# Performance work log

Measured on AMD Instinct MI355X. Metric: run time of the kernel, lower is better.

## Reference

```python
import jax, jax.numpy as jnp
import numpy as np

B, D = 65536, 365

def _linp(k, fan_in, fan_out):
    # torch nn.Linear default init: U(-1/sqrt(fan_in), 1/sqrt(fan_in))
    kw, kb = jax.random.split(k)
    bound = 1.0 / np.sqrt(fan_in)
    W = jax.random.uniform(kw, (fan_in, fan_out), jnp.float32, -bound, bound)
    b = jax.random.uniform(kb, (fan_out,), jnp.float32, -bound, bound)
    return W, b

def setup_inputs() -> dict:
    key = jax.random.key(0)
    ks = jax.random.split(key, 9)
    x = jax.random.normal(ks[0], (B, D), jnp.float32)
    W1, b1 = _linp(ks[1], D, 512)
    W2, b2 = _linp(ks[2], 512, 256)
    W3, b3 = _linp(ks[3], 256, 128)
    Ws, bs = _linp(ks[4], 6, 32)
    Wc1, bc1 = _linp(ks[5], 128 + 32, 64)
    Wc2, bc2 = _linp(ks[6], 64, 32)
    Wc3, bc3 = _linp(ks[7], 32, 1)
    return dict(x=x, W1=W1, b1=b1, W2=W2, b2=b2, W3=W3, b3=b3,
                Ws=Ws, bs=bs, Wc1=Wc1, bc1=bc1, Wc2=Wc2, bc2=bc2,
                Wc3=Wc3, bc3=bc3)

def _row_stats(x):
    # fused row-wise moments: mean, std (ddof=1), min, max, skew, kurtosis
    mu = jnp.mean(x, axis=1, keepdims=True)          # [B,1]
    c = x - mu                                        # [B,D]
    var1 = jnp.sum(c * c, axis=1) / (x.shape[1] - 1)  # unbiased, matches torch.std()
    sigma = jnp.sqrt(var1)
    m3 = jnp.mean(c ** 3, axis=1)
    m4 = jnp.mean(c ** 4, axis=1)
    skew = m3 / (sigma ** 3 + 1e-8)
    kurt = m4 / (sigma ** 4 + 1e-8)
    return jnp.stack([mu[:, 0], sigma, jnp.min(x, axis=1), jnp.max(x, axis=1), skew, kurt], axis=1)

def reference(x, W1, b1, W2, b2, W3, b3, Ws, bs, Wc1, bc1, Wc2, bc2, Wc3, bc3):
    h = jax.nn.relu(x @ W1 + b1)
    h = jax.nn.relu(h @ W2 + b2)
    seq = jax.nn.relu(h @ W3 + b3)            # [B,128]
    stat = _row_stats(x) @ Ws + bs            # [B,32]
    comb = jnp.concatenate([seq, stat], axis=1)
    c = jax.nn.relu(comb @ Wc1 + bc1)
    c = jax.nn.relu(c @ Wc2 + bc2)
    out = jax.nn.sigmoid(c @ Wc3 + bc3)       # [B,1]
    return out[:, 0]
```

## Files before the change

kernel.cpp:

```cpp
#include <hip/hip_runtime.h>
#include <math.h>

typedef __attribute__((ext_vector_type(8)))  short short8;
typedef __attribute__((ext_vector_type(16))) float float16;

#define DEVI __device__ __forceinline__

DEVI short f2bf(float f) {
    unsigned u = __float_as_uint(f);
    u = (u + 0x7fffu + ((u >> 16) & 1u)) >> 16;
    return (short)u;
}
DEVI unsigned pk2(float a, float b) {
    return (unsigned)(unsigned short)f2bf(a) | ((unsigned)(unsigned short)f2bf(b) << 16);
}
DEVI float16 mfma16(short8 a, short8 b, float16 c) {
    return __builtin_amdgcn_mfma_f32_32x32x16_bf16(a, b, c, 0, 0, 0);
}
DEVI int rowof(int r, int h) { return (r & 3) + 8 * (r >> 2) + 4 * h; }

__global__ void prep_weights(const float* __restrict__ W1, const float* __restrict__ W2,
                             const float* __restrict__ W3, const float* __restrict__ Wc1,
                             const float* __restrict__ Wc2, short* __restrict__ ws) {
    int idx = blockIdx.x * 256 + threadIdx.x;
    const float* src; int K, N, kpad, local, base;
    if (idx < 196608)      { base = 0;      local = idx;          K = 365; N = 512; kpad = 384; src = W1;  }
    else if (idx < 327680) { base = 196608; local = idx - 196608; K = 512; N = 256; kpad = 512; src = W2;  }
    else if (idx < 360448) { base = 327680; local = idx - 327680; K = 256; N = 128; kpad = 256; src = W3;  }
    else if (idx < 370688) { base = 360448; local = idx - 360448; K = 160; N = 64;  kpad = 160; src = Wc1; }
    else                   { base = 370688; local = idx - 370688; K = 64;  N = 32;  kpad = 64;  src = Wc2; }
    int n = local / kpad, kp = local - n * kpad;
    float v = (kp < K) ? src[kp * N + n] : 0.0f;
    ws[base + local] = f2bf(v);
}

__global__ __launch_bounds__(512, 2)
void fused_mlp(const float* __restrict__ x,
               const float* __restrict__ b1f, const float* __restrict__ b2f,
               const float* __restrict__ b3f, const float* __restrict__ Wsf,
               const float* __restrict__ bsf, const float* __restrict__ bc1f,
               const float* __restrict__ bc2f, const float* __restrict__ Wc3f,
               const float* __restrict__ bc3f,
               const short* __restrict__ W1t, const short* __restrict__ W2t,
               const short* __restrict__ W3t, const short* __restrict__ Wc1t,
               const short* __restrict__ Wc2t, float* __restrict__ out)
{
    __shared__ __align__(16) char smem[63488];
    short* AB0  = (short*)(smem);
    short* AB1  = (short*)(smem + 8192);
    short* SB0  = (short*)(smem + 16384);
    short* SB1  = (short*)(smem + 34816);
    short* C1s  = (short*)(smem + 16384);
    float* C2s  = (float*)(smem + 34816);
    short* FEAT = (short*)(smem + 53248);

    const int tid  = (int)threadIdx.x;
    const int lane = tid & 63;
    const int wave = tid >> 6;
    const int m    = lane & 31;
    const int h    = lane >> 5;
    const int rowBase = (int)blockIdx.x * 128;

    const int xr = tid >> 2;
    const int xo = (tid & 3) ^ (xr & 3);
    const float* xrow = x + (size_t)(rowBase + xr) * 365;

    float s1 = 0.f, s2 = 0.f, s3 = 0.f, s4 = 0.f, mn = 1e30f, mx = -1e30f;
    unsigned sxd[48];
    unsigned parkH1[64];
    unsigned park2[32];
    unsigned park3[16];

    auto issue_x = [&](int c, float* xf) {
        #pragma unroll
        for (int j = 0; j < 8; ++j) {
            int col = c * 32 + xo * 8 + j;
            xf[j] = (col < 365) ? xrow[col] : 0.f;
        }
    };
    auto mom_stash = [&](int c, const float* xf) {
        #pragma unroll
        for (int q = 0; q < 4; ++q) sxd[c * 4 + q] = pk2(xf[2 * q], xf[2 * q + 1]);
        #pragma unroll
        for (int j = 0; j < 8; ++j) {
            int col = c * 32 + xo * 8 + j;
            if (col < 365) {
                float v = xf[j], v2 = v * v;
                s1 += v; s2 += v2; s3 += v2 * v; s4 += v2 * v2;
                mn = fminf(mn, v); mx = fmaxf(mx, v);
            }
        }
    };
    auto write_a = [&](int c, short* A) {
        int4 w4;
        w4.x = (int)sxd[c * 4 + 0]; w4.y = (int)sxd[c * 4 + 1];
        w4.z = (int)sxd[c * 4 + 2]; w4.w = (int)sxd[c * 4 + 3];
        *(int4*)(A + tid * 8) = w4;
    };
    auto ldA = [&](const short* A, int mt, int ks) -> short8 {
        int a16 = (mt * 32 + m) * 4 + ((ks * 2 + h) ^ (m & 3));
        return *(const short8*)(A + a16 * 8);
    };
    auto ldS = [&](const short* S, int stride, int mt, int k0) -> short8 {
        return *(const short8*)(S + (mt * 32 + m) * stride + k0 + h * 8);
    };

    float16 A0, A1, A2, A3;
    #pragma unroll
    for (int i = 0; i < 16; ++i) { A0[i] = 0.f; A1[i] = 0.f; A2[i] = 0.f; A3[i] = 0.f; }
    float xfa[8], xfb[8];

    {
        const short* B1 = W1t + (wave * 32 + m) * 384 + h * 8;
        issue_x(0, xfa); issue_x(1, xfb);
        mom_stash(0, xfa);
        write_a(0, AB0);
        short8 bq0 = *(const short8*)(B1);
        short8 bq1 = *(const short8*)(B1 + 16);
        __syncthreads();
        #pragma unroll
        for (int c = 0; c < 12; ++c) {
            const short* Acur = (c & 1) ? AB1 : AB0;
            short*       Anxt = (c & 1) ? AB0 : AB1;
            if (c + 2 < 12) issue_x(c + 2, (c & 1) ? xfb : xfa);
            short8 nb0 = bq0, nb1 = bq1;
            if (c + 1 < 12) {
                nb0 = *(const short8*)(B1 + (c + 1) * 32);
                nb1 = *(const short8*)(B1 + (c + 1) * 32 + 16);
            }
            short8 a;
            a = ldA(Acur, 0, 0); A0 = mfma16(a, bq0, A0);
            a = ldA(Acur, 1, 0); A1 = mfma16(a, bq0, A1);
            a = ldA(Acur, 2, 0); A2 = mfma16(a, bq0, A2);
            a = ldA(Acur, 3, 0); A3 = mfma16(a, bq0, A3);
            a = ldA(Acur, 0, 1); A0 = mfma16(a, bq1, A0);
            a = ldA(Acur, 1, 1); A1 = mfma16(a, bq1, A1);
            a = ldA(Acur, 2, 1); A2 = mfma16(a, bq1, A2);
            a = ldA(Acur, 3, 1); A3 = mfma16(a, bq1, A3);
            if (c + 1 < 12) {
                mom_stash(c + 1, (c & 1) ? xfa : xfb);
                write_a(c + 1, Anxt);
            }
            bq0 = nb0; bq1 = nb1;
            __syncthreads();
        }
        float bb = b1f[wave * 32 + m];
        #pragma unroll
        for (int rr = 0; rr < 8; ++rr) {
            parkH1[rr]      = pk2(fmaxf(A0[2*rr] + bb, 0.f), fmaxf(A0[2*rr+1] + bb, 0.f));
            parkH1[8 + rr]  = pk2(fmaxf(A1[2*rr] + bb, 0.f), fmaxf(A1[2*rr+1] + bb, 0.f));
            parkH1[16 + rr] = pk2(fmaxf(A2[2*rr] + bb, 0.f), fmaxf(A2[2*rr+1] + bb, 0.f));
            parkH1[24 + rr] = pk2(fmaxf(A3[2*rr] + bb, 0.f), fmaxf(A3[2*rr+1] + bb, 0.f));
        }
    }

    {
        #pragma unroll
        for (int off = 1; off <= 2; off <<= 1) {
            s1 += __shfl_xor(s1, off); s2 += __shfl_xor(s2, off);
            s3 += __shfl_xor(s3, off); s4 += __shfl_xor(s4, off);
            mn = fminf(mn, __shfl_xor(mn, off)); mx = fmaxf(mx, __shfl_xor(mx, off));
        }
        float mean  = s1 * (1.0f / 365.0f);
        float var1  = (s2 - 365.0f * mean * mean) * (1.0f / 364.0f);
        float sigma = sqrtf(var1);
        float m3 = (s3 - 3.0f * mean * s2) * (1.0f / 365.0f) + 2.0f * mean * mean * mean;
        float mm = mean * mean;
        float m4 = (s4 - 4.0f * mean * s3 + 6.0f * mm * s2) * (1.0f / 365.0f) - 3.0f * mm * mm;
        float sg2 = sigma * sigma;
        float skew = m3 / (sigma * sg2 + 1e-8f);
        float kurt = m4 / (sg2 * sg2 + 1e-8f);
        float st[6] = { mean, sigma, mn, mx, skew, kurt };
        #pragma unroll
        for (int nn = 0; nn < 8; nn += 2) {
            int n0 = (tid & 3) * 8 + nn;
            float f0 = bsf[n0], f1 = bsf[n0 + 1];
            #pragma unroll
            for (int j = 0; j < 6; ++j) { f0 += st[j] * Wsf[j * 32 + n0]; f1 += st[j] * Wsf[j * 32 + n0 + 1]; }
            *(unsigned*)(FEAT + xr * 40 + n0) = pk2(f0, f1);
        }
    }

    {
        const short* B1 = W1t + ((8 + wave) * 32 + m) * 384 + h * 8;
        #pragma unroll
        for (int i = 0; i < 16; ++i) { A0[i] = 0.f; A1[i] = 0.f; A2[i] = 0.f; A3[i] = 0.f; }
        write_a(0, AB0);
        short8 bq0 = *(const short8*)(B1);
        short8 bq1 = *(const short8*)(B1 + 16);
        __syncthreads();
        #pragma unroll
        for (int c = 0; c < 12; ++c) {
            const short* Acur = (c & 1) ? AB1 : AB0;
            short*       Anxt = (c & 1) ? AB0 : AB1;
            short8 nb0 = bq0, nb1 = bq1;
            if (c + 1 < 12) {
                nb0 = *(const short8*)(B1 + (c + 1) * 32);
                nb1 = *(const short8*)(B1 + (c + 1) * 32 + 16);
            }
            short8 a;
            a = ldA(Acur, 0, 0); A0 = mfma16(a, bq0, A0);
            a = ldA(Acur, 1, 0); A1 = mfma16(a, bq0, A1);
            a = ldA(Acur, 2, 0); A2 = mfma16(a, bq0, A2);
            a = ldA(Acur, 3, 0); A3 = mfma16(a, bq0, A3);
            a = ldA(Acur, 0, 1); A0 = mfma16(a, bq1, A0);
            a = ldA(Acur, 1, 1); A1 = mfma16(a, bq1, A1);
            a = ldA(Acur, 2, 1); A2 = mfma16(a, bq1, A2);
            a = ldA(Acur, 3, 1); A3 = mfma16(a, bq1, A3);
            if (c + 1 < 12) write_a(c + 1, Anxt);
            bq0 = nb0; bq1 = nb1;
            __syncthreads();
        }
        float bb = b1f[(8 + wave) * 32 + m];
        #pragma unroll
        for (int rr = 0; rr < 8; ++rr) {
            parkH1[32 + rr]      = pk2(fmaxf(A0[2*rr] + bb, 0.f), fmaxf(A0[2*rr+1] + bb, 0.f));
            parkH1[32 + 8 + rr]  = pk2(fmaxf(A1[2*rr] + bb, 0.f), fmaxf(A1[2*rr+1] + bb, 0.f));
            parkH1[32 + 16 + rr] = pk2(fmaxf(A2[2*rr] + bb, 0.f), fmaxf(A2[2*rr+1] + bb, 0.f));
            parkH1[32 + 24 + rr] = pk2(fmaxf(A3[2*rr] + bb, 0.f), fmaxf(A3[2*rr+1] + bb, 0.f));
        }
    }

    float16 H0, H1, H2, H3;
    #pragma unroll
    for (int i = 0; i < 16; ++i) { H0[i] = 0.f; H1[i] = 0.f; H2[i] = 0.f; H3[i] = 0.f; }
    {
        const short* B2 = W2t + (wave * 32 + m) * 512 + h * 8;
        auto wS = [&](int c, short* S) {
            int lo = (2 * c) & 7;
            int pb = (c < 4) ? 0 : 32;
            if (wave == lo || wave == lo + 1) {
                int col = (wave - lo) * 32 + m;
                #pragma unroll
                for (int mt = 0; mt < 4; ++mt)
                #pragma unroll
                for (int rr = 0; rr < 8; ++rr) {
                    unsigned pv = parkH1[pb + mt * 8 + rr];
                    S[(mt * 32 + rowof(2 * rr,     h)) * 72 + col] = (short)(pv & 0xffffu);
                    S[(mt * 32 + rowof(2 * rr + 1, h)) * 72 + col] = (short)(pv >> 16);
                }
            }
        };
        wS(0, SB0);
        short8 cb[4], nb[4];
        #pragma unroll
        for (int ks = 0; ks < 4; ++ks) cb[ks] = *(const short8*)(B2 + ks * 16);
        __syncthreads();
        #pragma unroll
        for (int c = 0; c < 8; ++c) {
            const short* Scur = (c & 1) ? SB1 : SB0;
            short*       Snxt = (c & 1) ? SB0 : SB1;
            if (c + 1 < 8) {
                wS(c + 1, Snxt);
                #pragma unroll
                for (int ks = 0; ks < 4; ++ks) nb[ks] = *(const short8*)(B2 + (c + 1) * 64 + ks * 16);
            }
            #pragma unroll
            for (int ks = 0; ks < 4; ++ks) {
                short8 a;
                a = ldS(Scur, 72, 0, ks * 16); H0 = mfma16(a, cb[ks], H0);
                a = ldS(Scur, 72, 1, ks * 16); H1 = mfma16(a, cb[ks], H1);
                a = ldS(Scur, 72, 2, ks * 16); H2 = mfma16(a, cb[ks], H2);
                a = ldS(Scur, 72, 3, ks * 16); H3 = mfma16(a, cb[ks], H3);
            }
            if (c + 1 < 8) {
                #pragma unroll
                for (int ks = 0; ks < 4; ++ks) cb[ks] = nb[ks];
            }
            __syncthreads();
        }
        float bb = b2f[wave * 32 + m];
        #pragma unroll
        for (int rr = 0; rr < 8; ++rr) {
            park2[rr]      = pk2(fmaxf(H0[2*rr] + bb, 0.f), fmaxf(H0[2*rr+1] + bb, 0.f));
            park2[8 + rr]  = pk2(fmaxf(H1[2*rr] + bb, 0.f), fmaxf(H1[2*rr+1] + bb, 0.f));
            park2[16 + rr] = pk2(fmaxf(H2[2*rr] + bb, 0.f), fmaxf(H2[2*rr+1] + bb, 0.f));
            park2[24 + rr] = pk2(fmaxf(H3[2*rr] + bb, 0.f), fmaxf(H3[2*rr+1] + bb, 0.f));
        }
    }

    float16 Sq0, Sq1;
    #pragma unroll
    for (int i = 0; i < 16; ++i) { Sq0[i] = 0.f; Sq1[i] = 0.f; }
    {
        int nt3 = wave >> 1, mtb = 2 * (wave & 1);
        const short* B3 = W3t + (nt3 * 32 + m) * 256 + h * 8;
        auto wS3 = [&](int c, short* S) {
            int lo = 2 * c;
            if (wave == lo || wave == lo + 1) {
                int col = (wave - lo) * 32 + m;
                #pragma unroll
                for (int mt = 0; mt < 4; ++mt)
                #pragma unroll
                for (int rr = 0; rr < 8; ++rr) {
                    unsigned pv = park2[mt * 8 + rr];
                    S[(mt * 32 + rowof(2 * rr,     h)) * 72 + col] = (short)(pv & 0xffffu);
                    S[(mt * 32 + rowof(2 * rr + 1, h)) * 72 + col] = (short)(pv >> 16);
                }
            }
        };
        wS3(0, SB0);
        short8 cb[4], nb[4];
        #pragma unroll
        for (int ks = 0; ks < 4; ++ks) cb[ks] = *(const short8*)(B3 + ks * 16);
        __syncthreads();
        #pragma unroll
        for (int c = 0; c < 4; ++c) {
            const short* Scur = (c & 1) ? SB1 : SB0;
            short*       Snxt = (c & 1) ? SB0 : SB1;
            if (c + 1 < 4) {
                wS3(c + 1, Snxt);
                #pragma unroll
                for (int ks = 0; ks < 4; ++ks) nb[ks] = *(const short8*)(B3 + (c + 1) * 64 + ks * 16);
            }
            #pragma unroll
            for (int ks = 0; ks < 4; ++ks) {
                short8 a;
                a = ldS(Scur, 72, mtb,     ks * 16); Sq0 = mfma16(a, cb[ks], Sq0);
                a = ldS(Scur, 72, mtb + 1, ks * 16); Sq1 = mfma16(a, cb[ks], Sq1);
            }
            if (c + 1 < 4) {
                #pragma unroll
                for (int ks = 0; ks < 4; ++ks) cb[ks] = nb[ks];
            }
            __syncthreads();
        }
        float bb = b3f[nt3 * 32 + m];
        #pragma unroll
        for (int rr = 0; rr < 8; ++rr) {
            park3[rr]     = pk2(fmaxf(Sq0[2*rr] + bb, 0.f), fmaxf(Sq0[2*rr+1] + bb, 0.f));
            park3[8 + rr] = pk2(fmaxf(Sq1[2*rr] + bb, 0.f), fmaxf(Sq1[2*rr+1] + bb, 0.f));
        }
    }

    {
        int mt4 = wave & 3, nt4 = wave >> 2;
        const short* B4 = Wc1t + (nt4 * 32 + m) * 160 + h * 8;
        float bb = bc1f[nt4 * 32 + m];
        float16 Cv;
        #pragma unroll
        for (int i = 0; i < 16; ++i) Cv[i] = 0.f;
        auto wS4 = [&](int c, short* S) {
            if ((wave >> 2) == c) {
                int col = ((wave >> 1) & 1) * 32 + m;
                #pragma unroll
                for (int jj = 0; jj < 2; ++jj)
                #pragma unroll
                for (int rr = 0; rr < 8; ++rr) {
                    unsigned pv = park3[jj * 8 + rr];
                    int mt = 2 * (wave & 1) + jj;
                    S[(mt * 32 + rowof(2 * rr,     h)) * 72 + col] = (short)(pv & 0xffffu);
                    S[(mt * 32 + rowof(2 * rr + 1, h)) * 72 + col] = (short)(pv >> 16);
                }
            }
        };
        wS4(0, SB0); wS4(1, SB1);
        __syncthreads();
        #pragma unroll
        for (int ks = 0; ks < 4; ++ks) {
            short8 a = ldS(SB0, 72, mt4, ks * 16);
            short8 b = *(const short8*)(B4 + ks * 16);
            Cv = mfma16(a, b, Cv);
        }
        #pragma unroll
        for (int ks = 0; ks < 4; ++ks) {
            short8 a = ldS(SB1, 72, mt4, ks * 16);
            short8 b = *(const short8*)(B4 + 64 + ks * 16);
            Cv = mfma16(a, b, Cv);
        }
        #pragma unroll
        for (int ks = 0; ks < 2; ++ks) {
            short8 a = ldS(FEAT, 40, mt4, ks * 16);
            short8 b = *(const short8*)(B4 + 128 + ks * 16);
            Cv = mfma16(a, b, Cv);
        }
        __syncthreads();
        #pragma unroll
        for (int rr = 0; rr < 8; ++rr) {
            C1s[(mt4 * 32 + rowof(2 * rr,     h)) * 72 + nt4 * 32 + m] = f2bf(fmaxf(Cv[2*rr]   + bb, 0.f));
            C1s[(mt4 * 32 + rowof(2 * rr + 1, h)) * 72 + nt4 * 32 + m] = f2bf(fmaxf(Cv[2*rr+1] + bb, 0.f));
        }
        __syncthreads();
    }

    {
        if (wave < 4) {
            const short* B5 = Wc2t + m * 64 + h * 8;
            float bb = bc2f[m];
            float16 Cv;
            #pragma unroll
            for (int i = 0; i < 16; ++i) Cv[i] = 0.f;
            #pragma unroll
            for (int ks = 0; ks < 4; ++ks) {
                short8 a = ldS(C1s, 72, wave, ks * 16);
                short8 b = *(const short8*)(B5 + ks * 16);
                Cv = mfma16(a, b, Cv);
            }
            #pragma unroll
            for (int rr = 0; rr < 16; ++rr)
                C2s[(wave * 32 + rowof(rr, h)) * 33 + m] = fmaxf(Cv[rr] + bb, 0.f);
        }
        __syncthreads();
    }

    if (tid < 128) {
        float z = bc3f[0];
        #pragma unroll
        for (int i = 0; i < 32; ++i) z += C2s[tid * 33 + i] * Wc3f[i];
        out[rowBase + tid] = 1.0f / (1.0f + expf(-z));
    }
}

extern "C" void kernel_launch(void* const* d_in, const int* in_sizes, int n_in,
                              void* d_out, int out_size, void* d_ws, size_t ws_size,
                              hipStream_t stream)
{
    (void)in_sizes; (void)n_in; (void)out_size; (void)ws_size;
    const float* x   = (const float*)d_in[0];
    const float* W1  = (const float*)d_in[1];
    const float* b1  = (const float*)d_in[2];
    const float* W2  = (const float*)d_in[3];
    const float* b2  = (const float*)d_in[4];
    const float* W3  = (const float*)d_in[5];
    const float* b3  = (const float*)d_in[6];
    const float* Ws  = (const float*)d_in[7];
    const float* bs  = (const float*)d_in[8];
    const float* Wc1 = (const float*)d_in[9];
    const float* bc1 = (const float*)d_in[10];
    const float* Wc2 = (const float*)d_in[11];
    const float* bc2 = (const float*)d_in[12];
    const float* Wc3 = (const float*)d_in[13];
    const float* bc3 = (const float*)d_in[14];
    short* ws = (short*)d_ws;

    prep_weights<<<1456, 256, 0, stream>>>(W1, W2, W3, Wc1, Wc2, ws);
    fused_mlp<<<512, 512, 0, stream>>>(x, b1, b2, b3, Ws, bs, bc1, bc2, Wc3, bc3,
                                       ws, ws + 196608, ws + 327680, ws + 360448, ws + 370688,
                                       (float*)d_out);
}
```

Baseline: 238.2 us.

## Rewrite fused MLP with 64-row tiles, K-chunked weight layout, and interleaved layer streaming

Replaces the fused kernel with a new version that processes 64 rows per block instead of 128 and doubles the grid. The whole bf16 x tile is staged in LDS up front, and layer 1 and layer 2 are interleaved in 128-column slabs so hidden activations never need to be parked in registers. The weight prep kernel now writes a K-chunked (16-wide) transposed layout through an LDS transpose for coalesced stores. Occupancy is targeted higher via launch_bounds(512,4), at the cost of more redundant weight reads per row and more barriers.

```diff
diff --git a/kernel.cpp b/kernel.cpp
--- a/kernel.cpp
+++ b/kernel.cpp
@@ -18,149 +18,114 @@
     return __builtin_amdgcn_mfma_f32_32x32x16_bf16(a, b, c, 0, 0, 0);
 }
 DEVI int rowof(int r, int h) { return (r & 3) + 8 * (r >> 2) + 4 * h; }
-
-__global__ void prep_weights(const float* __restrict__ W1, const float* __restrict__ W2,
-                             const float* __restrict__ W3, const float* __restrict__ Wc1,
-                             const float* __restrict__ Wc2, short* __restrict__ ws) {
-    int idx = blockIdx.x * 256 + threadIdx.x;
-    const float* src; int K, N, kpad, local, base;
-    if (idx < 196608)      { base = 0;      local = idx;          K = 365; N = 512; kpad = 384; src = W1;  }
-    else if (idx < 327680) { base = 196608; local = idx - 196608; K = 512; N = 256; kpad = 512; src = W2;  }
-    else if (idx < 360448) { base = 327680; local = idx - 327680; K = 256; N = 128; kpad = 256; src = W3;  }
-    else if (idx < 370688) { base = 360448; local = idx - 360448; K = 160; N = 64;  kpad = 160; src = Wc1; }
-    else                   { base = 370688; local = idx - 370688; K = 64;  N = 32;  kpad = 64;  src = Wc2; }
-    int n = local / kpad, kp = local - n * kpad;
-    float v = (kp < K) ? src[kp * N + n] : 0.0f;
-    ws[base + local] = f2bf(v);
-}
-
-__global__ __launch_bounds__(512, 2)
-void fused_mlp(const float* __restrict__ x,
-               const float* __restrict__ b1f, const float* __restrict__ b2f,
-               const float* __restrict__ b3f, const float* __restrict__ Wsf,
-               const float* __restrict__ bsf, const float* __restrict__ bc1f,
-               const float* __restrict__ bc2f, const float* __restrict__ Wc3f,
-               const float* __restrict__ bc3f,
-               const short* __restrict__ W1t, const short* __restrict__ W2t,
-               const short* __restrict__ W3t, const short* __restrict__ Wc1t,
-               const short* __restrict__ Wc2t, float* __restrict__ out)
+DEVI short8 lds8(const short* p) { return *(const short8*)p; }
+
+#define W1T_OFF  0
+#define W2T_OFF  188416
+#define W3T_OFF  319488
+#define WC1T_OFF 352256
+#define WC2T_OFF 362496
+
+__global__ void prep_v2(const float* __restrict__ W1, const float* __restrict__ W2,
+                        const float* __restrict__ W3, const float* __restrict__ Wc1,
+                        const float* __restrict__ Wc2, short* __restrict__ ws) {
+    __shared__ short T[16 * 72];
+    int b = blockIdx.x, t = threadIdx.x;
+    const float* src; int K, N; size_t base; int kc, nb;
+    if (b < 184)        {            src = W1;  K = 365; N = 512; base = W1T_OFF;  kc = b >> 3;  nb = b & 7; }
+    else if (b < 312)   { int l = b - 184; src = W2;  K = 512; N = 256; base = W2T_OFF;  kc = l >> 2;  nb = l & 3; }
+    else if (b < 344)   { int l = b - 312; src = W3;  K = 256; N = 128; base = W3T_OFF;  kc = l >> 1;  nb = l & 1; }
+    else if (b < 354)   {            src = Wc1; K = 160; N = 64;  base = WC1T_OFF; kc = b - 344; nb = 0; }
+    else                {            src = Wc2; K = 64;  N = 32;  base = WC2T_OFF; kc = b - 354; nb = 0; }
+    int n = nb * 64 + (t & 63);
+    int kr = t >> 6;
+    #pragma unroll
+    for (int i = 0; i < 4; ++i) {
+        int krow = kr + 4 * i;
+        int k = kc * 16 + krow;
+        float v = (k < K && n < N) ? src[(size_t)k * N + n] : 0.f;
+        T[krow * 72 + (t & 63)] = f2bf(v);
+    }
+    __syncthreads();
+    int n2 = t >> 2, ksq = (t & 3) * 4;
+    int ng = nb * 64 + n2;
+    if (ng < N) {
+        unsigned lo = (unsigned)(unsigned short)T[ksq * 72 + n2]
+                    | ((unsigned)(unsigned short)T[(ksq + 1) * 72 + n2] << 16);
+        unsigned hi = (unsigned)(unsigned short)T[(ksq + 2) * 72 + n2]
+                    | ((unsigned)(unsigned short)T[(ksq + 3) * 72 + n2] << 16);
+        uint2 d; d.x = lo; d.y = hi;
+        *(uint2*)(ws + base + ((size_t)kc * N + ng) * 16 + ksq) = d;
+    }
+}
+
+__global__ __launch_bounds__(512, 4)
+void fused_v2(const float* __restrict__ x,
+              const float* __restrict__ b1f, const float* __restrict__ b2f,
+              const float* __restrict__ b3f, const float* __restrict__ Wsf,
+              const float* __restrict__ bsf, const float* __restrict__ bc1f,
+              const float* __restrict__ bc2f, const float* __restrict__ Wc3f,
+              const float* __restrict__ bc3f,
+              const short* __restrict__ wsw, float* __restrict__ out)
 {
-    __shared__ __align__(16) char smem[63488];
-    short* AB0  = (short*)(smem);
-    short* AB1  = (short*)(smem + 8192);
-    short* SB0  = (short*)(smem + 16384);
-    short* SB1  = (short*)(smem + 34816);
-    short* C1s  = (short*)(smem + 16384);
-    float* C2s  = (float*)(smem + 34816);
-    short* FEAT = (short*)(smem + 53248);
+    __shared__ __align__(16) char smem[65536];
+    short* XT    = (short*)smem;
+    short* SB    = (short*)(smem + 48128);
+    short* C1    = (short*)smem;
+    short* FEATL = (short*)(smem + 12288);
+    float* C2    = (float*)(smem + 20480);
+
+    const short* W1t  = wsw + W1T_OFF;
+    const short* W2t  = wsw + W2T_OFF;
+    const short* W3t  = wsw + W3T_OFF;
+    const short* Wc1t = wsw + WC1T_OFF;
+    const short* Wc2t = wsw + WC2T_OFF;
 
     const int tid  = (int)threadIdx.x;
     const int lane = tid & 63;
-    const int wave = tid >> 6;
+    const int wv   = tid >> 6;
     const int m    = lane & 31;
     const int h    = lane >> 5;
-    const int rowBase = (int)blockIdx.x * 128;
-
-    const int xr = tid >> 2;
-    const int xo = (tid & 3) ^ (xr & 3);
-    const float* xrow = x + (size_t)(rowBase + xr) * 365;
-
+    const int mt   = wv & 1;
+    const int nl   = wv >> 1;
+    const int rowBase = (int)blockIdx.x * 64;
+
+    const int r0 = tid >> 3, j0 = tid & 7;
+    const float* xrow = x + (size_t)(rowBase + r0) * 365;
     float s1 = 0.f, s2 = 0.f, s3 = 0.f, s4 = 0.f, mn = 1e30f, mx = -1e30f;
-    unsigned sxd[48];
-    unsigned parkH1[64];
-    unsigned park2[32];
-    unsigned park3[16];
-
-    auto issue_x = [&](int c, float* xf) {
-        #pragma unroll
-        for (int j = 0; j < 8; ++j) {
-            int col = c * 32 + xo * 8 + j;
-            xf[j] = (col < 365) ? xrow[col] : 0.f;
-        }
-    };
-    auto mom_stash = [&](int c, const float* xf) {
-        #pragma unroll
-        for (int q = 0; q < 4; ++q) sxd[c * 4 + q] = pk2(xf[2 * q], xf[2 * q + 1]);
-        #pragma unroll
-        for (int j = 0; j < 8; ++j) {
-            int col = c * 32 + xo * 8 + j;
-            if (col < 365) {
-                float v = xf[j], v2 = v * v;
-                s1 += v; s2 += v2; s3 += v2 * v; s4 += v2 * v2;
-                mn = fminf(mn, v); mx = fmaxf(mx, v);
-            }
-        }
-    };
-    auto write_a = [&](int c, short* A) {
-        int4 w4;
-        w4.x = (int)sxd[c * 4 + 0]; w4.y = (int)sxd[c * 4 + 1];
-        w4.z = (int)sxd[c * 4 + 2]; w4.w = (int)sxd[c * 4 + 3];
-        *(int4*)(A + tid * 8) = w4;
-    };
-    auto ldA = [&](const short* A, int mt, int ks) -> short8 {
-        int a16 = (mt * 32 + m) * 4 + ((ks * 2 + h) ^ (m & 3));
-        return *(const short8*)(A + a16 * 8);
-    };
-    auto ldS = [&](const short* S, int stride, int mt, int k0) -> short8 {
-        return *(const short8*)(S + (mt * 32 + m) * stride + k0 + h * 8);
-    };
-
-    float16 A0, A1, A2, A3;
-    #pragma unroll
-    for (int i = 0; i < 16; ++i) { A0[i] = 0.f; A1[i] = 0.f; A2[i] = 0.f; A3[i] = 0.f; }
-    float xfa[8], xfb[8];
-
+    #pragma unroll
+    for (int i = 0; i < 6; ++i) {
+        int o = j0 + 8 * i;
+        if (o <= 45) {
+            float xf[8];
+            #pragma unroll
+            for (int jj = 0; jj < 8; ++jj) {
+                int col = o * 8 + jj;
+                xf[jj] = (col < 365) ? xrow[col] : 0.f;
+            }
+            #pragma unroll
+            for (int jj = 0; jj < 8; ++jj) {
+                int col = o * 8 + jj;
+                if (col < 365) {
+                    float v = xf[jj], v2 = v * v;
+                    s1 += v; s2 += v2; s3 += v2 * v; s4 += v2 * v2;
+                    mn = fminf(mn, v); mx = fmaxf(mx, v);
+                }
+            }
+            int4 w4;
+            w4.x = (int)pk2(xf[0], xf[1]); w4.y = (int)pk2(xf[2], xf[3]);
+            w4.z = (int)pk2(xf[4], xf[5]); w4.w = (int)pk2(xf[6], xf[7]);
+            *(int4*)(XT + r0 * 376 + o * 8) = w4;
+        }
+    }
+    #pragma unroll
+    for (int off = 1; off <= 4; off <<= 1) {
+        s1 += __shfl_xor(s1, off); s2 += __shfl_xor(s2, off);
+        s3 += __shfl_xor(s3, off); s4 += __shfl_xor(s4, off);
+        mn = fminf(mn, __shfl_xor(mn, off)); mx = fmaxf(mx, __shfl_xor(mx, off));
+    }
+    unsigned fdw0, fdw1;
     {
-        const short* B1 = W1t + (wave * 32 + m) * 384 + h * 8;
-        issue_x(0, xfa); issue_x(1, xfb);
-        mom_stash(0, xfa);
-        write_a(0, AB0);
-        short8 bq0 = *(const short8*)(B1);
-        short8 bq1 = *(const short8*)(B1 + 16);
-        __syncthreads();
-        #pragma unroll
-        for (int c = 0; c < 12; ++c) {
-            const short* Acur = (c & 1) ? AB1 : AB0;
-            short*       Anxt = (c & 1) ? AB0 : AB1;
-            if (c + 2 < 12) issue_x(c + 2, (c & 1) ? xfb : xfa);
-            short8 nb0 = bq0, nb1 = bq1;
-            if (c + 1 < 12) {
-                nb0 = *(const short8*)(B1 + (c + 1) * 32);
-                nb1 = *(const short8*)(B1 + (c + 1) * 32 + 16);
-            }
-            short8 a;
-            a = ldA(Acur, 0, 0); A0 = mfma16(a, bq0, A0);
-            a = ldA(Acur, 1, 0); A1 = mfma16(a, bq0, A1);
-            a = ldA(Acur, 2, 0); A2 = mfma16(a, bq0, A2);
-            a = ldA(Acur, 3, 0); A3 = mfma16(a, bq0, A3);
-            a = ldA(Acur, 0, 1); A0 = mfma16(a, bq1, A0);
-            a = ldA(Acur, 1, 1); A1 = mfma16(a, bq1, A1);
-            a = ldA(Acur, 2, 1); A2 = mfma16(a, bq1, A2);
-            a = ldA(Acur, 3, 1); A3 = mfma16(a, bq1, A3);
-            if (c + 1 < 12) {
-                mom_stash(c + 1, (c & 1) ? xfa : xfb);
-                write_a(c + 1, Anxt);
-            }
-            bq0 = nb0; bq1 = nb1;
-            __syncthreads();
-        }
-        float bb = b1f[wave * 32 + m];
-        #pragma unroll
-        for (int rr = 0; rr < 8; ++rr) {
-            parkH1[rr]      = pk2(fmaxf(A0[2*rr] + bb, 0.f), fmaxf(A0[2*rr+1] + bb, 0.f));
-            parkH1[8 + rr]  = pk2(fmaxf(A1[2*rr] + bb, 0.f), fmaxf(A1[2*rr+1] + bb, 0.f));
-            parkH1[16 + rr] = pk2(fmaxf(A2[2*rr] + bb, 0.f), fmaxf(A2[2*rr+1] + bb, 0.f));
-            parkH1[24 + rr] = pk2(fmaxf(A3[2*rr] + bb, 0.f), fmaxf(A3[2*rr+1] + bb, 0.f));
-        }
-    }
-
-    {
-        #pragma unroll
-        for (int off = 1; off <= 2; off <<= 1) {
-            s1 += __shfl_xor(s1, off); s2 += __shfl_xor(s2, off);
-            s3 += __shfl_xor(s3, off); s4 += __shfl_xor(s4, off);
-            mn = fminf(mn, __shfl_xor(mn, off)); mx = fmaxf(mx, __shfl_xor(mx, off));
-        }
         float mean  = s1 * (1.0f / 365.0f);
         float var1  = (s2 - 365.0f * mean * mean) * (1.0f / 364.0f);
         float sigma = sqrtf(var1);
@@ -171,242 +136,163 @@
         float skew = m3 / (sigma * sg2 + 1e-8f);
         float kurt = m4 / (sg2 * sg2 + 1e-8f);
         float st[6] = { mean, sigma, mn, mx, skew, kurt };
-        #pragma unroll
-        for (int nn = 0; nn < 8; nn += 2) {
-            int n0 = (tid & 3) * 8 + nn;
-            float f0 = bsf[n0], f1 = bsf[n0 + 1];
-            #pragma unroll
-            for (int j = 0; j < 6; ++j) { f0 += st[j] * Wsf[j * 32 + n0]; f1 += st[j] * Wsf[j * 32 + n0 + 1]; }
-            *(unsigned*)(FEAT + xr * 40 + n0) = pk2(f0, f1);
-        }
-    }
-
+        float f[4];
+        #pragma unroll
+        for (int c0 = 0; c0 < 4; ++c0) {
+            int c = 4 * j0 + c0;
+            float acc = bsf[c];
+            #pragma unroll
+            for (int jj = 0; jj < 6; ++jj) acc += st[jj] * Wsf[jj * 32 + c];
+            f[c0] = acc;
+        }
+        fdw0 = pk2(f[0], f[1]); fdw1 = pk2(f[2], f[3]);
+    }
+    __syncthreads();
+
+    float16 h2a0, h2a1;
+    #pragma unroll
+    for (int i = 0; i < 16; ++i) { h2a0[i] = 0.f; h2a1[i] = 0.f; }
+
+    const short* Ap = XT + (mt * 32 + m) * 376 + h * 8;
+
+    for (int p = 0; p < 2; ++p) {
+        float16 ga0, ga1;
+        #pragma unroll
+        for (int i = 0; i < 16; ++i) { ga0[i] = 0.f; ga1[i] = 0.f; }
+        int nc0 = 256 * p + 32 * nl;
+        const short* Bp0 = W1t + (nc0 + m) * 16 + h * 8;
+        const short* Bp1 = Bp0 + 128 * 16;
+        #pragma unroll
+        for (int kc = 0; kc < 23; ++kc) {
+            short8 a  = lds8(Ap + kc * 16);
+            short8 b0 = *(const short8*)(Bp0 + kc * 8192);
+            short8 b1 = *(const short8*)(Bp1 + kc * 8192);
+            ga0 = mfma16(a, b0, ga0);
+            ga1 = mfma16(a, b1, ga1);
+        }
+        #pragma unroll
+        for (int q = 0; q < 2; ++q) {
+            __syncthreads();
+            {
+                int nc = 256 * p + 128 * q + 32 * nl;
+                float bb = b1f[nc + m];
+                float16 A;
+                if (q) A = ga1; else A = ga0;
+                #pragma unroll
+                for (int r = 0; r < 16; ++r) {
+                    int rw = mt * 32 + rowof(r, h);
+                    SB[rw * 136 + 32 * nl + m] = f2bf(fmaxf(A[r] + bb, 0.f));
+                }
+            }
+            __syncthreads();
+            int slab = 2 * p + q;
+            const short* A2p  = SB + (mt * 32 + m) * 136 + h * 8;
+            const short* B2p0 = W2t + (size_t)slab * 8 * 4096 + (32 * nl + m) * 16 + h * 8;
+            const short* B2p1 = B2p0 + 128 * 16;
+            #pragma unroll
+            for (int i = 0; i < 8; ++i) {
+                short8 a  = lds8(A2p + i * 16);
+                short8 b0 = *(const short8*)(B2p0 + i * 4096);
+                short8 b1 = *(const short8*)(B2p1 + i * 4096);
+                h2a0 = mfma16(a, b0, h2a0);
+                h2a1 = mfma16(a, b1, h2a1);
+            }
+        }
+    }
+
+    float16 g3a;
+    #pragma unroll
+    for (int i = 0; i < 16; ++i) g3a[i] = 0.f;
+    for (int s = 0; s < 2; ++s) {
+        __syncthreads();
+        {
+            float bb = b2f[32 * nl + 128 * s + m];
+            float16 A;
+            if (s) A = h2a1; else A = h2a0;
+            #pragma unroll
+            for (int r = 0; r < 16; ++r) {
+                int rw = mt * 32 + rowof(r, h);
+                SB[rw * 136 + 32 * nl + m] = f2bf(fmaxf(A[r] + bb, 0.f));
+            }
+        }
+        __syncthreads();
+        const short* A3p = SB + (mt * 32 + m) * 136 + h * 8;
+        const short* B3p = W3t + (size_t)s * 8 * 2048 + (32 * nl + m) * 16 + h * 8;
+        #pragma unroll
+        for (int i = 0; i < 8; ++i) {
+            short8 a = lds8(A3p + i * 16);
+            short8 b = *(const short8*)(B3p + i * 2048);
+            g3a = mfma16(a, b, g3a);
+        }
+    }
+
+    __syncthreads();
     {
-        const short* B1 = W1t + ((8 + wave) * 32 + m) * 384 + h * 8;
-        #pragma unroll
-        for (int i = 0; i < 16; ++i) { A0[i] = 0.f; A1[i] = 0.f; A2[i] = 0.f; A3[i] = 0.f; }
-        write_a(0, AB0);
-        short8 bq0 = *(const short8*)(B1);
-        short8 bq1 = *(const short8*)(B1 + 16);
-        __syncthreads();
-        #pragma unroll
-        for (int c = 0; c < 12; ++c) {
-            const short* Acur = (c & 1) ? AB1 : AB0;
-            short*       Anxt = (c & 1) ? AB0 : AB1;
-            short8 nb0 = bq0, nb1 = bq1;
-            if (c + 1 < 12) {
-                nb0 = *(const short8*)(B1 + (c + 1) * 32);
-                nb1 = *(const short8*)(B1 + (c + 1) * 32 + 16);
-            }
-            short8 a;
-            a = ldA(Acur, 0, 0); A0 = mfma16(a, bq0, A0);
-            a = ldA(Acur, 1, 0); A1 = mfma16(a, bq0, A1);
-            a = ldA(Acur, 2, 0); A2 = mfma16(a, bq0, A2);
-            a = ldA(Acur, 3, 0); A3 = mfma16(a, bq0, A3);
-            a = ldA(Acur, 0, 1); A0 = mfma16(a, bq1, A0);
-            a = ldA(Acur, 1, 1); A1 = mfma16(a, bq1, A1);
-            a = ldA(Acur, 2, 1); A2 = mfma16(a, bq1, A2);
-            a = ldA(Acur, 3, 1); A3 = mfma16(a, bq1, A3);
-            if (c + 1 < 12) write_a(c + 1, Anxt);
-            bq0 = nb0; bq1 = nb1;
-            __syncthreads();
-        }
-        float bb = b1f[(8 + wave) * 32 + m];
-        #pragma unroll
-        for (int rr = 0; rr < 8; ++rr) {
-            parkH1[32 + rr]      = pk2(fmaxf(A0[2*rr] + bb, 0.f), fmaxf(A0[2*rr+1] + bb, 0.f));
-            parkH1[32 + 8 + rr]  = pk2(fmaxf(A1[2*rr] + bb, 0.f), fmaxf(A1[2*rr+1] + bb, 0.f));
-            parkH1[32 + 16 + rr] = pk2(fmaxf(A2[2*rr] + bb, 0.f), fmaxf(A2[2*rr+1] + bb, 0.f));
-            parkH1[32 + 24 + rr] = pk2(fmaxf(A3[2*rr] + bb, 0.f), fmaxf(A3[2*rr+1] + bb, 0.f));
-        }
-    }
-
-    float16 H0, H1, H2, H3;
-    #pragma unroll
-    for (int i = 0; i < 16; ++i) { H0[i] = 0.f; H1[i] = 0.f; H2[i] = 0.f; H3[i] = 0.f; }
-    {
-        const short* B2 = W2t + (wave * 32 + m) * 512 + h * 8;
-        auto wS = [&](int c, short* S) {
-            int lo = (2 * c) & 7;
-            int pb = (c < 4) ? 0 : 32;
-            if (wave == lo || wave == lo + 1) {
-                int col = (wave - lo) * 32 + m;
-                #pragma unroll
-                for (int mt = 0; mt < 4; ++mt)
-                #pragma unroll
-                for (int rr = 0; rr < 8; ++rr) {
-                    unsigned pv = parkH1[pb + mt * 8 + rr];
-                    S[(mt * 32 + rowof(2 * rr,     h)) * 72 + col] = (short)(pv & 0xffffu);
-                    S[(mt * 32 + rowof(2 * rr + 1, h)) * 72 + col] = (short)(pv >> 16);
-                }
-            }
-        };
-        wS(0, SB0);
-        short8 cb[4], nb[4];
-        #pragma unroll
-        for (int ks = 0; ks < 4; ++ks) cb[ks] = *(const short8*)(B2 + ks * 16);
-        __syncthreads();
-        #pragma unroll
-        for (int c = 0; c < 8; ++c) {
-            const short* Scur = (c & 1) ? SB1 : SB0;
-            short*       Snxt = (c & 1) ? SB0 : SB1;
-            if (c + 1 < 8) {
-                wS(c + 1, Snxt);
-                #pragma unroll
-                for (int ks = 0; ks < 4; ++ks) nb[ks] = *(const short8*)(B2 + (c + 1) * 64 + ks * 16);
-            }
-            #pragma unroll
-            for (int ks = 0; ks < 4; ++ks) {
-                short8 a;
-                a = ldS(Scur, 72, 0, ks * 16); H0 = mfma16(a, cb[ks], H0);
-                a = ldS(Scur, 72, 1, ks * 16); H1 = mfma16(a, cb[ks], H1);
-                a = ldS(Scur, 72, 2, ks * 16); H2 = mfma16(a, cb[ks], H2);
-                a = ldS(Scur, 72, 3, ks * 16); H3 = mfma16(a, cb[ks], H3);
-            }
-            if (c + 1 < 8) {
-                #pragma unroll
-                for (int ks = 0; ks < 4; ++ks) cb[ks] = nb[ks];
-            }
-            __syncthreads();
-        }
-        float bb = b2f[wave * 32 + m];
-        #pragma unroll
-        for (int rr = 0; rr < 8; ++rr) {
-            park2[rr]      = pk2(fmaxf(H0[2*rr] + bb, 0.f), fmaxf(H0[2*rr+1] + bb, 0.f));
-            park2[8 + rr]  = pk2(fmaxf(H1[2*rr] + bb, 0.f), fmaxf(H1[2*rr+1] + bb, 0.f));
-            park2[16 + rr] = pk2(fmaxf(H2[2*rr] + bb, 0.f), fmaxf(H2[2*rr+1] + bb, 0.f));
-            park2[24 + rr] = pk2(fmaxf(H3[2*rr] + bb, 0.f), fmaxf(H3[2*rr+1] + bb, 0.f));
-        }
-    }
-
-    float16 Sq0, Sq1;
-    #pragma unroll
-    for (int i = 0; i < 16; ++i) { Sq0[i] = 0.f; Sq1[i] = 0.f; }
-    {
-        int nt3 = wave >> 1, mtb = 2 * (wave & 1);
-        const short* B3 = W3t + (nt3 * 32 + m) * 256 + h * 8;
-        auto wS3 = [&](int c, short* S) {
-            int lo = 2 * c;
-            if (wave == lo || wave == lo + 1) {
-                int col = (wave - lo) * 32 + m;
-                #pragma unroll
-                for (int mt = 0; mt < 4; ++mt)
-                #pragma unroll
-                for (int rr = 0; rr < 8; ++rr) {
-                    unsigned pv = park2[mt * 8 + rr];
-                    S[(mt * 32 + rowof(2 * rr,     h)) * 72 + col] = (short)(pv & 0xffffu);
-                    S[(mt * 32 + rowof(2 * rr + 1, h)) * 72 + col] = (short)(pv >> 16);
-                }
-            }
-        };
-        wS3(0, SB0);
-        short8 cb[4], nb[4];
-        #pragma unroll
-        for (int ks = 0; ks < 4; ++ks) cb[ks] = *(const short8*)(B3 + ks * 16);
-        __syncthreads();
-        #pragma unroll
-        for (int c = 0; c < 4; ++c) {
-            const short* Scur = (c & 1) ? SB1 : SB0;
-            short*       Snxt = (c & 1) ? SB0 : SB1;
-            if (c + 1 < 4) {
-                wS3(c + 1, Snxt);
-                #pragma unroll
-                for (int ks = 0; ks < 4; ++ks) nb[ks] = *(const short8*)(B3 + (c + 1) * 64 + ks * 16);
-            }
-            #pragma unroll
-            for (int ks = 0; ks < 4; ++ks) {
-                short8 a;
-                a = ldS(Scur, 72, mtb,     ks * 16); Sq0 = mfma16(a, cb[ks], Sq0);
-                a = ldS(Scur, 72, mtb + 1, ks * 16); Sq1 = mfma16(a, cb[ks], Sq1);
-            }
-            if (c + 1 < 4) {
-                #pragma unroll
-                for (int ks = 0; ks < 4; ++ks) cb[ks] = nb[ks];
-            }
-            __syncthreads();
-        }
-        float bb = b3f[nt3 * 32 + m];
-        #pragma unroll
-        for (int rr = 0; rr < 8; ++rr) {
-            park3[rr]     = pk2(fmaxf(Sq0[2*rr] + bb, 0.f), fmaxf(Sq0[2*rr+1] + bb, 0.f));
-            park3[8 + rr] = pk2(fmaxf(Sq1[2*rr] + bb, 0.f), fmaxf(Sq1[2*rr+1] + bb, 0.f));
-        }
-    }
-
-    {
-        int mt4 = wave & 3, nt4 = wave >> 2;
-        const short* B4 = Wc1t + (nt4 * 32 + m) * 160 + h * 8;
-        float bb = bc1f[nt4 * 32 + m];
-        float16 Cv;
-        #pragma unroll
-        for (int i = 0; i < 16; ++i) Cv[i] = 0.f;
-        auto wS4 = [&](int c, short* S) {
-            if ((wave >> 2) == c) {
-                int col = ((wave >> 1) & 1) * 32 + m;
-                #pragma unroll
-                for (int jj = 0; jj < 2; ++jj)
-                #pragma unroll
-                for (int rr = 0; rr < 8; ++rr) {
-                    unsigned pv = park3[jj * 8 + rr];
-                    int mt = 2 * (wave & 1) + jj;
-                    S[(mt * 32 + rowof(2 * rr,     h)) * 72 + col] = (short)(pv & 0xffffu);
-                    S[(mt * 32 + rowof(2 * rr + 1, h)) * 72 + col] = (short)(pv >> 16);
-                }
-            }
-        };
-        wS4(0, SB0); wS4(1, SB1);
-        __syncthreads();
-        #pragma unroll
-        for (int ks = 0; ks < 4; ++ks) {
-            short8 a = ldS(SB0, 72, mt4, ks * 16);
-            short8 b = *(const short8*)(B4 + ks * 16);
-            Cv = mfma16(a, b, Cv);
-        }
-        #pragma unroll
-        for (int ks = 0; ks < 4; ++ks) {
-            short8 a = ldS(SB1, 72, mt4, ks * 16);
-            short8 b = *(const short8*)(B4 + 64 + ks * 16);
-            Cv = mfma16(a, b, Cv);
-        }
-        #pragma unroll
-        for (int ks = 0; ks < 2; ++ks) {
-            short8 a = ldS(FEAT, 40, mt4, ks * 16);
-            short8 b = *(const short8*)(B4 + 128 + ks * 16);
-            Cv = mfma16(a, b, Cv);
-        }
-        __syncthreads();
-        #pragma unroll
-        for (int rr = 0; rr < 8; ++rr) {
-            C1s[(mt4 * 32 + rowof(2 * rr,     h)) * 72 + nt4 * 32 + m] = f2bf(fmaxf(Cv[2*rr]   + bb, 0.f));
-            C1s[(mt4 * 32 + rowof(2 * rr + 1, h)) * 72 + nt4 * 32 + m] = f2bf(fmaxf(Cv[2*rr+1] + bb, 0.f));
-        }
-        __syncthreads();
-    }
-
-    {
-        if (wave < 4) {
-            const short* B5 = Wc2t + m * 64 + h * 8;
-            float bb = bc2f[m];
-            float16 Cv;
-            #pragma unroll
-            for (int i = 0; i < 16; ++i) Cv[i] = 0.f;
-            #pragma unroll
-            for (int ks = 0; ks < 4; ++ks) {
-                short8 a = ldS(C1s, 72, wave, ks * 16);
-                short8 b = *(const short8*)(B5 + ks * 16);
-                Cv = mfma16(a, b, Cv);
-            }
-            #pragma unroll
-            for (int rr = 0; rr < 16; ++rr)
-                C2s[(wave * 32 + rowof(rr, h)) * 33 + m] = fmaxf(Cv[rr] + bb, 0.f);
-        }
-        __syncthreads();
-    }
-
-    if (tid < 128) {
+        float bb = b3f[32 * nl + m];
+        #pragma unroll
+        for (int r = 0; r < 16; ++r) {
+            int rw = mt * 32 + rowof(r, h);
+            SB[rw * 136 + 32 * nl + m] = f2bf(fmaxf(g3a[r] + bb, 0.f));
+        }
+        *(unsigned*)(FEATL + r0 * 40 + 4 * j0)     = fdw0;
+        *(unsigned*)(FEATL + r0 * 40 + 4 * j0 + 2) = fdw1;
+    }
+    __syncthreads();
+
+    if (wv < 4) {
+        int nt4 = wv >> 1;
+        float16 g4a;
+        #pragma unroll
+        for (int i = 0; i < 16; ++i) g4a[i] = 0.f;
+        const short* A4p = SB + (mt * 32 + m) * 136 + h * 8;
+        const short* B4p = Wc1t + (32 * nt4 + m) * 16 + h * 8;
+        #pragma unroll
+        for (int i = 0; i < 8; ++i) {
+            short8 a = lds8(A4p + i * 16);
+            short8 b = *(const short8*)(B4p + i * 1024);
+            g4a = mfma16(a, b, g4a);
+        }
+        const short* AF = FEATL + (mt * 32 + m) * 40 + h * 8;
+        #pragma unroll
+        for (int i = 0; i < 2; ++i) {
+            short8 a = lds8(AF + i * 16);
+            short8 b = *(const short8*)(B4p + (8 + i) * 1024);
+            g4a = mfma16(a, b, g4a);
+        }
+        float bb = bc1f[32 * nt4 + m];
+        #pragma unroll
+        for (int r = 0; r < 16; ++r) {
+            int rw = mt * 32 + rowof(r, h);
+            C1[rw * 72 + 32 * nt4 + m] = f2bf(fmaxf(g4a[r] + bb, 0.f));
+        }
+    }
+    __syncthreads();
+
+    if (wv < 2) {
+        float16 g5;
+        #pragma unroll
+        for (int i = 0; i < 16; ++i) g5[i] = 0.f;
+        const short* A5p = C1 + (wv * 32 + m) * 72 + h * 8;
+        const short* B5p = Wc2t + m * 16 + h * 8;
+        #pragma unroll
+        for (int i = 0; i < 4; ++i) {
+            short8 a = lds8(A5p + i * 16);
+            short8 b = *(const short8*)(B5p + i * 512);
+            g5 = mfma16(a, b, g5);
+        }
+        float bb = bc2f[m];
+        #pragma unroll
+        for (int r = 0; r < 16; ++r) {
+            int rw = wv * 32 + rowof(r, h);
+            C2[rw * 33 + m] = fmaxf(g5[r] + bb, 0.f);
+        }
+    }
+    __syncthreads();
+
+    if (tid < 64) {
         float z = bc3f[0];
         #pragma unroll
-        for (int i = 0; i < 32; ++i) z += C2s[tid * 33 + i] * Wc3f[i];
+        for (int i = 0; i < 32; ++i) z += C2[tid * 33 + i] * Wc3f[i];
         out[rowBase + tid] = 1.0f / (1.0f + expf(-z));
     }
 }
@@ -433,8 +319,7 @@
     const float* bc3 = (const float*)d_in[14];
     short* ws = (short*)d_ws;
 
-    prep_weights<<<1456, 256, 0, stream>>>(W1, W2, W3, Wc1, Wc2, ws);
-    fused_mlp<<<512, 512, 0, stream>>>(x, b1, b2, b3, Ws, bs, bc1, bc2, Wc3, bc3,
-                                       ws, ws + 196608, ws + 327680, ws + 360448, ws + 370688,
-                                       (float*)d_out);
-}
+    prep_v2<<<358, 256, 0, stream>>>(W1, W2, W3, Wc1, Wc2, ws);
+    fused_v2<<<1024, 512, 0, stream>>>(x, b1, b2, b3, Ws, bs, bc1, bc2, Wc3, bc3,
+                                       ws, (float*)d_out);
+}
```

New measurement: 237.5 us. Within noise of the previous version (-0.3%).
